# Optimization experiments

Hardware: AMD Instinct MI355X
Metric: run time of the kernel (lower is better)

Reference implementation:

```python
import jax, jax.numpy as jnp
from jax import lax
import numpy as np


def conv2d(x, w, b):
    # x: NCHW, w: OIHW, VALID padding, stride 1
    y = lax.conv_general_dilated(x, w, (1, 1), 'VALID',
                                 dimension_numbers=('NCHW', 'OIHW', 'NCHW'))
    return y + b[None, :, None, None]


def prelu(x, a):
    # per-channel PReLU, a: (C,)
    return jnp.where(x >= 0, x, a[None, :, None, None] * x)


def maxpool_ceil(x, k, s):
    # max pool with ceil_mode=True: pad right/bottom with -inf as needed
    H, W = x.shape[2], x.shape[3]
    def pad_amt(n):
        out = -(-(n - k) // s) + 1  # ceil
        return max(0, (out - 1) * s + k - n)
    ph, pw = pad_amt(H), pad_amt(W)
    return lax.reduce_window(x, -jnp.inf, lax.max,
                             (1, 1, k, k), (1, 1, s, s),
                             ((0, 0), (0, 0), (0, ph), (0, pw)))


def setup_inputs() -> dict:
    key = jax.random.key(0)
    ks = jax.random.split(key, 24)
    N = 2048
    x = jax.random.normal(ks[0], (N, 3, 48, 48), dtype=jnp.float32)

    def w_init(k, shape, fan_in):
        return jax.random.normal(k, shape, dtype=jnp.float32) * (1.0 / np.sqrt(fan_in))

    inp = {'x': x}
    inp['c1w'] = w_init(ks[1], (32, 3, 3, 3), 3 * 9)
    inp['c1b'] = jnp.zeros((32,), jnp.float32)
    inp['a1'] = jax.random.uniform(ks[2], (32,), jnp.float32, 0.1, 0.4)
    inp['c2w'] = w_init(ks[3], (64, 32, 3, 3), 32 * 9)
    inp['c2b'] = jnp.zeros((64,), jnp.float32)
    inp['a2'] = jax.random.uniform(ks[4], (64,), jnp.float32, 0.1, 0.4)
    inp['c3w'] = w_init(ks[5], (64, 64, 3, 3), 64 * 9)
    inp['c3b'] = jnp.zeros((64,), jnp.float32)
    inp['a3'] = jax.random.uniform(ks[6], (64,), jnp.float32, 0.1, 0.4)
    inp['c4w'] = w_init(ks[7], (128, 64, 2, 2), 64 * 4)
    inp['c4b'] = jnp.zeros((128,), jnp.float32)
    inp['a4'] = jax.random.uniform(ks[8], (128,), jnp.float32, 0.1, 0.4)
    inp['d5w'] = w_init(ks[9], (256, 1152), 1152)
    inp['d5b'] = jnp.zeros((256,), jnp.float32)
    inp['a5'] = jax.random.uniform(ks[10], (256,), jnp.float32, 0.1, 0.4)
    inp['d61w'] = w_init(ks[11], (2, 256), 256)
    inp['d61b'] = jnp.zeros((2,), jnp.float32)
    inp['d62w'] = w_init(ks[12], (4, 256), 256)
    inp['d62b'] = jnp.zeros((4,), jnp.float32)
    inp['d63w'] = w_init(ks[13], (10, 256), 256)
    inp['d63b'] = jnp.zeros((10,), jnp.float32)
    return inp


def reference(x, c1w, c1b, a1, c2w, c2b, a2, c3w, c3b, a3, c4w, c4b, a4,
              d5w, d5b, a5, d61w, d61b, d62w, d62b, d63w, d63b):
    h = prelu(conv2d(x, c1w, c1b), a1)          # [N,32,46,46]
    h = maxpool_ceil(h, 3, 2)                   # [N,32,23,23]
    h = prelu(conv2d(h, c2w, c2b), a2)          # [N,64,21,21]
    h = maxpool_ceil(h, 3, 2)                   # [N,64,10,10]
    h = prelu(conv2d(h, c3w, c3b), a3)          # [N,64,8,8]
    h = maxpool_ceil(h, 2, 2)                   # [N,64,4,4]
    h = prelu(conv2d(h, c4w, c4b), a4)          # [N,128,3,3]
    # torch: x.permute(0,3,2,1).contiguous().view(N,-1)
    h = jnp.transpose(h, (0, 3, 2, 1)).reshape(h.shape[0], -1)  # [N,1152]
    h = h @ d5w.T + d5b                         # [N,256]
    h = jnp.where(h >= 0, h, a5 * h)            # PReLU over features
    a = jax.nn.softmax(h @ d61w.T + d61b, axis=1)  # class probs [N,2]
    b = h @ d62w.T + d62b
    c = h @ d63w.T + d63b                       # landmarks [N,10]
    return (b, c, a)
```

## Files before the change

### kernel.cpp

```cpp
#include <hip/hip_runtime.h>
#include <hip/hip_bf16.h>
#include <hip/hip_fp16.h>
#include <stdint.h>

typedef short s16x8 __attribute__((ext_vector_type(8)));
typedef unsigned short u16x8 __attribute__((ext_vector_type(8)));
typedef _Float16 f16x8 __attribute__((ext_vector_type(8)));
typedef __fp16 h16x2 __attribute__((ext_vector_type(2)));
typedef float f32x4 __attribute__((ext_vector_type(4)));

__device__ __forceinline__ unsigned short f2h(float f) {
    __half h = __float2half(f);
    union { __half h; unsigned short u; } c; c.h = h; return c.u;
}
__device__ __forceinline__ float h2f(unsigned short u) {
    union { unsigned short u; __half h; } c; c.u = u; return __half2float(c.h);
}
__device__ __forceinline__ unsigned pkh(float a, float b) {
    union { h16x2 h; unsigned u; } c;
    c.h = __builtin_amdgcn_cvt_pkrtz(a, b);
    return c.u;
}

__global__ void k0_prep(const float* __restrict__ c2w, const float* __restrict__ c3w,
                        const float* __restrict__ c4w, const float* __restrict__ d5w,
                        unsigned short* __restrict__ w2, unsigned short* __restrict__ w3,
                        unsigned short* __restrict__ w4, unsigned short* __restrict__ w5) {
    int t = blockIdx.x * 256 + threadIdx.x;
    if (t < 18432) {
        int kpos = t / 2048, rem = t % 2048, oc = rem / 32, ic = rem % 32;
        w2[t] = f2h(c2w[(oc * 32 + ic) * 9 + kpos]);
        return;
    }
    t -= 18432;
    if (t < 36864) {
        int kpos = t / 4096, rem = t % 4096, oc = rem / 64, ic = rem % 64;
        w3[t] = f2h(c3w[(oc * 64 + ic) * 9 + kpos]);
        return;
    }
    t -= 36864;
    if (t < 32768) {
        int kpos = t / 8192, rem = t % 8192, oc = rem / 64, ic = rem % 64;
        w4[t] = f2h(c4w[(oc * 64 + ic) * 4 + kpos]);
        return;
    }
    t -= 32768;
    if (t < 294912) w5[t] = f2h(d5w[t]);
}

__global__ __launch_bounds__(256, 6)
void k1_conv1(const float* __restrict__ x, const float* __restrict__ c1w,
              const float* __restrict__ c1b, const float* __restrict__ a1,
              unsigned short* __restrict__ p1) {
    __shared__ unsigned short xstrip[1008];
    __shared__ unsigned short cbuf[230 * 40];
    __shared__ unsigned short wlds[1024];
    __shared__ float bls[32], als[32];

    const int n = blockIdx.x, tid = threadIdx.x;
    const int w = tid >> 6, lane = tid & 63, q = lane >> 4, l16 = lane & 15;

    for (int t = tid; t < 1024; t += 256) {
        int oc = t >> 5, k = t & 31;
        wlds[t] = (k < 27) ? f2h(c1w[oc * 27 + k]) : (unsigned short)0;
    }
    if (tid < 32) { bls[tid] = c1b[tid]; als[tid] = a1[tid]; }
    __syncthreads();

    f16x8 Wf[2];
    #pragma unroll
    for (int nt = 0; nt < 2; ++nt) {
        union { u16x8 u; f16x8 f; } cc;
        cc.u = *(const u16x8*)(wlds + (nt * 16 + l16) * 32 + q * 8);
        Wf[nt] = cc.f;
    }

    float bq[2][4], aq[2][4];
    #pragma unroll
    for (int nt = 0; nt < 2; ++nt)
    #pragma unroll
    for (int r = 0; r < 4; ++r) {
        bq[nt][r] = bls[nt * 16 + q * 4 + r];
        aq[nt][r] = als[nt * 16 + q * 4 + r];
    }

    int off[8];
    #pragma unroll
    for (int j = 0; j < 8; ++j) {
        int k = q * 8 + j;
        int kk = k < 27 ? k : 26;
        int ic = kk / 9, r9 = kk - ic * 9, ky = r9 / 3, kx = r9 - ky * 3;
        off[j] = ic * 336 + ky * 48 + kx;
    }

    auto do_pool = [&](int sp, int nprows, int kymax) {
        int ntask = nprows * 92;
        int t = tid;
        if (t < ntask) {
            int ocg = t & 3; unsigned r2 = (unsigned)t >> 2;
            int px = (int)(r2 % 23u), py_l = (int)(r2 / 23u);
            int kxmax = (px == 22) ? 2 : 3;
            int base = (2 * py_l * 46 + 2 * px) * 40 + ocg * 8;
            f16x8 mx;
            #pragma unroll
            for (int j = 0; j < 8; ++j) mx[j] = (_Float16)(-60000.f);
            #pragma unroll
            for (int ky = 0; ky < 3; ++ky) {
                if (ky < kymax) {
                    #pragma unroll
                    for (int kx = 0; kx < 3; ++kx) {
                        if (kx < kxmax) {
                            union { uint4 u; f16x8 f; } d;
                            d.u = *(const uint4*)&cbuf[base + (ky * 46 + kx) * 40];
                            mx = __builtin_elementwise_max(mx, d.f);
                        }
                    }
                }
            }
            union { f16x8 f; uint4 u; } o; o.f = mx;
            int py = 2 * sp + py_l;
            *(uint4*)&p1[n * 16928 + (py * 23 + px) * 32 + ocg * 8] = o.u;
        }
    };

    for (int s = 0; s < 12; ++s) {
        const int nrows = (s == 11) ? 2 : 5;
        const int P = 46 * nrows;
        const int ntiles = (P + 15) >> 4;
        const int xr0 = 4 * s;

        {
            int t4 = tid;
            if (t4 < 252) {
                int ic = t4 / 84;
                int rem4 = t4 * 4 - ic * 336;
                int rr = rem4 / 48, col = rem4 - rr * 48;
                int row = xr0 + rr; if (row > 47) row = 47;
                float4 f = *(const float4*)(x + n * 6912 + ic * 2304 + row * 48 + col);
                uint2 o; o.x = pkh(f.x, f.y); o.y = pkh(f.z, f.w);
                *(uint2*)&xstrip[t4 * 4] = o;
            }
        }
        if (s > 0) do_pool(s - 1, 2, 3);
        __syncthreads();

        for (int T = w; T < ntiles; T += 4) {
            int px = T * 16 + l16;
            int p = px < P ? px : P - 1;
            int ry = p / 46, cx = p - ry * 46;
            int basex = ry * 48 + cx;
            union { u16x8 u; f16x8 f; } xcc;
            #pragma unroll
            for (int j = 0; j < 8; ++j) xcc.u[j] = xstrip[basex + off[j]];
            f16x8 Xf = xcc.f;
            f32x4 acc[2] = {{0.f,0.f,0.f,0.f},{0.f,0.f,0.f,0.f}};
            #pragma unroll
            for (int nt = 0; nt < 2; ++nt)
                acc[nt] = __builtin_amdgcn_mfma_f32_16x16x32_f16(Wf[nt], Xf, acc[nt], 0, 0, 0);
            if (px < P) {
                #pragma unroll
                for (int nt = 0; nt < 2; ++nt) {
                    float v0 = acc[nt][0] + bq[nt][0];
                    float v1 = acc[nt][1] + bq[nt][1];
                    float v2 = acc[nt][2] + bq[nt][2];
                    float v3 = acc[nt][3] + bq[nt][3];
                    v0 = fmaxf(v0, 0.f) + aq[nt][0] * fminf(v0, 0.f);
                    v1 = fmaxf(v1, 0.f) + aq[nt][1] * fminf(v1, 0.f);
                    v2 = fmaxf(v2, 0.f) + aq[nt][2] * fminf(v2, 0.f);
                    v3 = fmaxf(v3, 0.f) + aq[nt][3] * fminf(v3, 0.f);
                    uint2 pk; pk.x = pkh(v0, v1); pk.y = pkh(v2, v3);
                    *(uint2*)&cbuf[px * 40 + nt * 16 + q * 4] = pk;
                }
            }
        }
        __syncthreads();
    }
    do_pool(11, 1, 2);
}

__global__ __launch_bounds__(256, 2)
void k23_fused(const unsigned short* __restrict__ p1, const unsigned short* __restrict__ w2,
               const float* __restrict__ c2b, const float* __restrict__ a2,
               const unsigned short* __restrict__ w3, const float* __restrict__ c3b,
               const float* __restrict__ a3, const unsigned short* __restrict__ w4,
               const float* __restrict__ c4b, const float* __restrict__ a4,
               unsigned short* __restrict__ flat) {
    __shared__ __align__(16) char smem[52128];
    unsigned short* xs    = (unsigned short*)(smem);
    unsigned short* c2s   = (unsigned short*)(smem + 16560);
    unsigned short* p2s   = (unsigned short*)(smem + 37728);
    unsigned short* c3buf = (unsigned short*)(smem);
    unsigned short* p3    = (unsigned short*)(smem + 8192);

    const int n = blockIdx.x, tid = threadIdx.x;
    const int w = tid >> 6, lane = tid & 63, q = lane >> 4, l16 = lane & 15;
    const unsigned short* p1n = p1 + n * 16928;

    const int npair = w & 1, tset = w >> 1;
    const int ocA = npair * 32 + l16, ocB = npair * 32 + 16 + l16;

    f16x8 B2[9][2];
    #pragma unroll
    for (int kp = 0; kp < 9; ++kp) {
        union { u16x8 u; f16x8 f; } c0, c1;
        c0.u = *(const u16x8*)(w2 + (kp * 64 + ocA) * 32 + q * 8);
        c1.u = *(const u16x8*)(w2 + (kp * 64 + ocB) * 32 + q * 8);
        B2[kp][0] = c0.f; B2[kp][1] = c1.f;
    }
    const float b2a = c2b[ocA], b2b = c2b[ocB];
    const float a2a = a2[ocA],  a2b = a2[ocB];

    auto stage = [&](int s) {
        int pr0 = 6 * s;
        for (int t = tid; t < 828; t += 256) {
            int pxl = t >> 2, c = t & 3;
            int rr = pxl / 23, colpx = pxl - rr * 23;
            int prow = pr0 + rr; if (prow > 22) prow = 22;
            uint4 d = ((const uint4*)p1n)[(prow * 23 + colpx) * 4 + c];
            ((uint4*)xs)[pxl * 5 + c] = d;
        }
    };

    auto conv2_strip = [&](int s) {
        const int nr = (s == 3) ? 3 : 7;
        const int P = 21 * nr;
        const int ntiles = (P + 15) >> 4;
        const int half = (ntiles + 1) >> 1;
        const int T0 = tset * half;
        const int T1 = (T0 + half) < ntiles ? (T0 + half) : ntiles;
        for (int T = T0; T < T1; ++T) {
            int m = T * 16 + l16;
            int p = m < P ? m : P - 1;
            int ry = p / 21, ox = p - ry * 21;
            const unsigned short* ab = xs + (ry * 23 + ox) * 40 + q * 8;
            f32x4 acc0 = {0.f, 0.f, 0.f, 0.f}, acc1 = {0.f, 0.f, 0.f, 0.f};
            #pragma unroll
            for (int kp = 0; kp < 9; ++kp) {
                int ky = kp / 3, kx = kp - ky * 3;
                union { u16x8 u; f16x8 f; } av;
                av.u = *(const u16x8*)(ab + (ky * 23 + kx) * 40);
                acc0 = __builtin_amdgcn_mfma_f32_16x16x32_f16(av.f, B2[kp][0], acc0, 0, 0, 0);
                acc1 = __builtin_amdgcn_mfma_f32_16x16x32_f16(av.f, B2[kp][1], acc1, 0, 0, 0);
            }
            int rowb = T * 16 + q * 4;
            #pragma unroll
            for (int r = 0; r < 4; ++r) {
                int row = rowb + r;
                if (row < P) {
                    float v0 = acc0[r] + b2a;
                    v0 = fmaxf(v0, 0.f) + a2a * fminf(v0, 0.f);
                    c2s[row * 72 + npair * 32 + l16] = f2h(v0);
                    float v1 = acc1[r] + b2b;
                    v1 = fmaxf(v1, 0.f) + a2b * fminf(v1, 0.f);
                    c2s[row * 72 + npair * 32 + 16 + l16] = f2h(v1);
                }
            }
        }
    };

    auto pool_strip = [&](int s) {
        int nprow = (s == 3) ? 1 : 3;
        int ntask = nprow * 80;
        if (tid < ntask) {
            int ocg = tid & 7; int r2 = tid >> 3;
            int px = r2 % 10, pyl = r2 / 10;
            int base = (2 * pyl * 21 + 2 * px) * 72 + ocg * 8;
            f16x8 mx;
            #pragma unroll
            for (int j = 0; j < 8; ++j) mx[j] = (_Float16)(-60000.f);
            #pragma unroll
            for (int ky = 0; ky < 3; ++ky)
            #pragma unroll
            for (int kx = 0; kx < 3; ++kx) {
                union { uint4 u; f16x8 f; } d;
                d.u = *(const uint4*)&c2s[base + (ky * 21 + kx) * 72];
                mx = __builtin_elementwise_max(mx, d.f);
            }
            union { f16x8 f; uint4 u; } o; o.f = mx;
            *(uint4*)&p2s[((3 * s + pyl) * 10 + px) * 72 + ocg * 8] = o.u;
        }
    };

    stage(0);
    __syncthreads();
    for (int s = 0; s < 4; ++s) {
        conv2_strip(s);
        __syncthreads();
        pool_strip(s);
        if (s < 3) stage(s + 1);
        __syncthreads();
    }

    {
        const int oc3 = w * 16 + l16;
        int mbase[4];
        #pragma unroll
        for (int j = 0; j < 4; ++j) {
            int px = j * 16 + l16;
            int oy = px >> 3, ox = px & 7;
            mbase[j] = (oy * 10 + ox) * 72 + q * 8;
        }
        f32x4 acc3[4];
        #pragma unroll
        for (int j = 0; j < 4; ++j) acc3[j] = f32x4{0.f, 0.f, 0.f, 0.f};
        union { u16x8 u; f16x8 f; } bc;
        bc.u = *(const u16x8*)(w3 + oc3 * 64 + q * 8);
        f16x8 B3c = bc.f;
        for (int c = 0; c < 18; ++c) {
            f16x8 B3n = B3c;
            if (c < 17) {
                int cn = c + 1;
                union { u16x8 u; f16x8 f; } bn;
                bn.u = *(const u16x8*)(w3 + ((cn >> 1) * 64 + oc3) * 64 + (cn & 1) * 32 + q * 8);
                B3n = bn.f;
            }
            int kp = c >> 1, ky = kp / 3, kx = kp - ky * 3;
            int aoff = (ky * 10 + kx) * 72 + (c & 1) * 32;
            #pragma unroll
            for (int j = 0; j < 4; ++j) {
                union { u16x8 u; f16x8 f; } av;
                av.u = *(const u16x8*)(p2s + mbase[j] + aoff);
                acc3[j] = __builtin_amdgcn_mfma_f32_16x16x32_f16(av.f, B3c, acc3[j], 0, 0, 0);
            }
            B3c = B3n;
        }
        float bias = c3b[oc3], al = a3[oc3];
        #pragma unroll
        for (int j = 0; j < 4; ++j)
        #pragma unroll
        for (int r = 0; r < 4; ++r) {
            int row = j * 16 + q * 4 + r;
            float val = acc3[j][r] + bias;
            val = fmaxf(val, 0.f) + al * fminf(val, 0.f);
            c3buf[row * 64 + oc3] = f2h(val);
        }
    }
    __syncthreads();

    if (tid < 128) {
        int ocg = tid & 7, r = tid >> 3;
        int py = r >> 2, pxo = r & 3;
        f16x8 mx;
        #pragma unroll
        for (int j = 0; j < 8; ++j) mx[j] = (_Float16)(-60000.f);
        #pragma unroll
        for (int ky = 0; ky < 2; ++ky)
        #pragma unroll
        for (int kx = 0; kx < 2; ++kx) {
            union { uint4 u; f16x8 f; } d;
            d.u = *(const uint4*)&c3buf[((py * 2 + ky) * 8 + pxo * 2 + kx) * 64 + ocg * 8];
            mx = __builtin_elementwise_max(mx, d.f);
        }
        union { f16x8 f; uint4 u; } o; o.f = mx;
        *(uint4*)&p3[r * 72 + ocg * 8] = o.u;
    }
    __syncthreads();

    {
        int px = l16 < 9 ? l16 : 8;
        int oy = px / 3, ox = px - oy * 3;
        const int mb4 = (oy * 4 + ox) * 72 + q * 8;
        const int oc4a = (w * 2) * 16 + l16, oc4b = (w * 2 + 1) * 16 + l16;
        f32x4 acc4[2] = {{0.f,0.f,0.f,0.f},{0.f,0.f,0.f,0.f}};
        f16x8 B4c[2];
        {
            union { u16x8 u; f16x8 f; } b0, b1;
            b0.u = *(const u16x8*)(w4 + oc4a * 64 + q * 8);
            b1.u = *(const u16x8*)(w4 + oc4b * 64 + q * 8);
            B4c[0] = b0.f; B4c[1] = b1.f;
        }
        for (int c = 0; c < 8; ++c) {
            f16x8 B4n[2] = {B4c[0], B4c[1]};
            if (c < 7) {
                int cn = c + 1;
                int boff = (cn >> 1) * 8192 + (cn & 1) * 32 + q * 8;
                union { u16x8 u; f16x8 f; } b0, b1;
                b0.u = *(const u16x8*)(w4 + boff + oc4a * 64);
                b1.u = *(const u16x8*)(w4 + boff + oc4b * 64);
                B4n[0] = b0.f; B4n[1] = b1.f;
            }
            int kp = c >> 1, ky = kp >> 1, kx = kp & 1;
            union { u16x8 u; f16x8 f; } av;
            av.u = *(const u16x8*)(p3 + mb4 + (ky * 4 + kx) * 72 + (c & 1) * 32);
            acc4[0] = __builtin_amdgcn_mfma_f32_16x16x32_f16(av.f, B4c[0], acc4[0], 0, 0, 0);
            acc4[1] = __builtin_amdgcn_mfma_f32_16x16x32_f16(av.f, B4c[1], acc4[1], 0, 0, 0);
            B4c[0] = B4n[0]; B4c[1] = B4n[1];
        }
        #pragma unroll
        for (int h = 0; h < 2; ++h) {
            int oc = h ? oc4b : oc4a;
            float bias = c4b[oc], al = a4[oc];
            #pragma unroll
            for (int r = 0; r < 4; ++r) {
                int row = q * 4 + r;
                if (row < 9) {
                    int hy = row / 3, wx = row - hy * 3;
                    float val = acc4[h][r] + bias;
                    val = fmaxf(val, 0.f) + al * fminf(val, 0.f);
                    flat[(unsigned)n * 1152u + (wx * 3 + hy) * 128 + oc] = f2h(val);
                }
            }
        }
    }
}

__global__ __launch_bounds__(256, 2)
void k5a_gemm(const unsigned short* __restrict__ flat, const unsigned short* __restrict__ w5,
              const float* __restrict__ d5b, const float* __restrict__ a5,
              unsigned short* __restrict__ h) {
    __shared__ float hbuf[4 * 16 * 128];
    const int blk = blockIdx.x, tid = threadIdx.x;
    const int w = tid >> 6, lane = tid & 63, q = lane >> 4, l16 = lane & 15;
    const int img0 = (blk >> 1) * 16, ocb = (blk & 1) * 128;
    const int img = img0 + l16;

    f32x4 acc[8];
    #pragma unroll
    for (int nt = 0; nt < 8; ++nt) acc[nt] = f32x4{0.f, 0.f, 0.f, 0.f};

    for (int cc = 0; cc < 9; ++cc) {
        int c = w * 9 + cc;
        int k0 = c * 32 + q * 8;
        union { u16x8 u; f16x8 f; } av;
        av.u = *(const u16x8*)(flat + (unsigned)img * 1152u + k0);
        #pragma unroll
        for (int nt = 0; nt < 8; ++nt) {
            int oc = ocb + nt * 16 + l16;
            union { u16x8 u; f16x8 f; } bv;
            bv.u = *(const u16x8*)(w5 + (unsigned)oc * 1152u + k0);
            acc[nt] = __builtin_amdgcn_mfma_f32_16x16x32_f16(av.f, bv.f, acc[nt], 0, 0, 0);
        }
    }
    #pragma unroll
    for (int nt = 0; nt < 8; ++nt)
    #pragma unroll
    for (int r = 0; r < 4; ++r) {
        int row = q * 4 + r;
        hbuf[(w * 16 + row) * 128 + nt * 16 + l16] = acc[nt][r];
    }
    __syncthreads();
    for (int t = tid; t < 1024; t += 256) {
        int im = t >> 6, oc2 = (t & 63) * 2;
        float s0 = hbuf[im * 128 + oc2]        + hbuf[(16 + im) * 128 + oc2]
                 + hbuf[(32 + im) * 128 + oc2] + hbuf[(48 + im) * 128 + oc2];
        float s1 = hbuf[im * 128 + oc2 + 1]        + hbuf[(16 + im) * 128 + oc2 + 1]
                 + hbuf[(32 + im) * 128 + oc2 + 1] + hbuf[(48 + im) * 128 + oc2 + 1];
        int oc = ocb + oc2;
        s0 += d5b[oc];     s0 = fmaxf(s0, 0.f) + a5[oc] * fminf(s0, 0.f);
        s1 += d5b[oc + 1]; s1 = fmaxf(s1, 0.f) + a5[oc + 1] * fminf(s1, 0.f);
        *(unsigned*)&h[(unsigned)(img0 + im) * 256u + oc] = pkh(s0, s1);
    }
}

__global__ __launch_bounds__(256, 2)
void k5b_head(const unsigned short* __restrict__ h,
              const float* __restrict__ d61w, const float* __restrict__ d61b,
              const float* __restrict__ d62w, const float* __restrict__ d62b,
              const float* __restrict__ d63w, const float* __restrict__ d63b,
              float* __restrict__ out) {
    __shared__ float hL[16 * 260];
    __shared__ float wl[16 * 260];
    __shared__ float lg[256];
    const int blk = blockIdx.x, tid = threadIdx.x;
    const int img0 = blk * 16;

    for (int t = tid; t < 512; t += 256) {
        int im = t >> 5, g = t & 31;
        union { uint4 u; f16x8 f; } d;
        d.u = *(const uint4*)&h[(unsigned)(img0 + im) * 256u + g * 8];
        float* dst = &hL[im * 260 + g * 8];
        #pragma unroll
        for (int j = 0; j < 8; ++j) dst[j] = (float)d.f[j];
    }
    {
        int o = tid >> 4, seg = tid & 15;
        const float* wrow = (o < 2) ? d61w + o * 256
                          : (o < 6) ? d62w + (o - 2) * 256
                          :           d63w + (o - 6) * 256;
        #pragma unroll
        for (int j = 0; j < 4; ++j)
            *(float4*)&wl[o * 260 + seg * 16 + j * 4] = ((const float4*)wrow)[seg * 4 + j];
    }
    __syncthreads();

    const int im = tid >> 4, o = tid & 15;
    {
        float bias = (o < 2) ? d61b[o] : (o < 6) ? d62b[o - 2] : d63b[o - 6];
        float s = bias;
        const float4* ha = (const float4*)&hL[im * 260];
        const float4* wa = (const float4*)&wl[o * 260];
        #pragma unroll 8
        for (int k = 0; k < 64; ++k) {
            float4 a = ha[k], b = wa[k];
            s += a.x * b.x + a.y * b.y + a.z * b.z + a.w * b.w;
        }
        lg[im * 16 + o] = s;
    }
    __syncthreads();
    {
        int gimg = img0 + im;
        float v = lg[im * 16 + o];
        if (o >= 2 && o < 6) {
            out[gimg * 4 + (o - 2)] = v;
        } else if (o >= 6) {
            out[8192 + gimg * 10 + (o - 6)] = v;
        } else {
            float l0 = lg[im * 16 + 0], l1 = lg[im * 16 + 1];
            float mx = fmaxf(l0, l1);
            float e0 = __expf(l0 - mx), e1 = __expf(l1 - mx);
            out[28672 + gimg * 2 + o] = (o == 0 ? e0 : e1) / (e0 + e1);
        }
    }
}

extern "C" void kernel_launch(void* const* d_in, const int* in_sizes, int n_in,
                              void* d_out, int out_size, void* d_ws, size_t ws_size,
                              hipStream_t stream) {
    (void)in_sizes; (void)n_in; (void)out_size; (void)ws_size;
    const float* x    = (const float*)d_in[0];
    const float* c1w  = (const float*)d_in[1];
    const float* c1b  = (const float*)d_in[2];
    const float* a1   = (const float*)d_in[3];
    const float* c2w  = (const float*)d_in[4];
    const float* c2b  = (const float*)d_in[5];
    const float* a2   = (const float*)d_in[6];
    const float* c3w  = (const float*)d_in[7];
    const float* c3b  = (const float*)d_in[8];
    const float* a3   = (const float*)d_in[9];
    const float* c4w  = (const float*)d_in[10];
    const float* c4b  = (const float*)d_in[11];
    const float* a4   = (const float*)d_in[12];
    const float* d5w  = (const float*)d_in[13];
    const float* d5b  = (const float*)d_in[14];
    const float* a5   = (const float*)d_in[15];
    const float* d61w = (const float*)d_in[16];
    const float* d61b = (const float*)d_in[17];
    const float* d62w = (const float*)d_in[18];
    const float* d62b = (const float*)d_in[19];
    const float* d63w = (const float*)d_in[20];
    const float* d63b = (const float*)d_in[21];

    char* ws = (char*)d_ws;
    unsigned short* p1    = (unsigned short*)(ws + 0);
    unsigned short* flat  = (unsigned short*)(ws + 69337088);
    unsigned short* h     = (unsigned short*)(ws + 74055680);
    unsigned short* w2    = (unsigned short*)(ws + 186777600);
    unsigned short* w3    = (unsigned short*)(ws + 186814464);
    unsigned short* w4    = (unsigned short*)(ws + 186888192);
    unsigned short* w5    = (unsigned short*)(ws + 186953728);

    k0_prep  <<<1496, 256, 0, stream>>>(c2w, c3w, c4w, d5w, w2, w3, w4, w5);
    k1_conv1 <<<2048, 256, 0, stream>>>(x, c1w, c1b, a1, p1);
    k23_fused<<<2048, 256, 0, stream>>>(p1, w2, c2b, a2, w3, c3b, a3, w4, c4b, a4, flat);
    k5a_gemm <<<256, 256, 0, stream>>>(flat, w5, d5b, a5, h);
    k5b_head <<<128, 256, 0, stream>>>(h, d61w, d61b, d62w, d62b, d63w, d63b,
                                       (float*)d_out);
}
```

Measured before the change: 296.9 us.

## Fuse dense GEMM into head kernel and shrink conv2 strip shared memory

The dense-5 GEMM and the head are merged into one kernel. Each block now computes all 256 outputs for 16 images with a full K loop, applies bias and PReLU, and writes to shared memory directly, which removes the global h buffer and one launch. In the conv2 stage, the padded strides (40, 72) become unpadded (32, 64), and the loop runs 5 strips of 5 rows instead of 4 strips of 7. This cuts shared memory so more blocks fit per CU and lets staging become a plain contiguous copy, at the risk of LDS bank conflicts. The fused kernel runs only 128 blocks with a long serial K loop, so it may underutilize the GPU.

```diff
diff --git a/kernel.cpp b/kernel.cpp
--- a/kernel.cpp
+++ b/kernel.cpp
@@ -12,9 +12,6 @@
 __device__ __forceinline__ unsigned short f2h(float f) {
     __half h = __float2half(f);
     union { __half h; unsigned short u; } c; c.h = h; return c.u;
-}
-__device__ __forceinline__ float h2f(unsigned short u) {
-    union { unsigned short u; __half h; } c; c.u = u; return __half2float(c.h);
 }
 __device__ __forceinline__ unsigned pkh(float a, float b) {
     union { h16x2 h; unsigned u; } c;
@@ -185,10 +182,10 @@
                const float* __restrict__ a3, const unsigned short* __restrict__ w4,
                const float* __restrict__ c4b, const float* __restrict__ a4,
                unsigned short* __restrict__ flat) {
-    __shared__ __align__(16) char smem[52128];
+    __shared__ __align__(16) char smem[36544];
     unsigned short* xs    = (unsigned short*)(smem);
-    unsigned short* c2s   = (unsigned short*)(smem + 16560);
-    unsigned short* p2s   = (unsigned short*)(smem + 37728);
+    unsigned short* c2s   = (unsigned short*)(smem + 10304);
+    unsigned short* p2s   = (unsigned short*)(smem + 23744);
     unsigned short* c3buf = (unsigned short*)(smem);
     unsigned short* p3    = (unsigned short*)(smem + 8192);
 
@@ -211,34 +208,25 @@
     const float a2a = a2[ocA],  a2b = a2[ocB];
 
     auto stage = [&](int s) {
-        int pr0 = 6 * s;
-        for (int t = tid; t < 828; t += 256) {
-            int pxl = t >> 2, c = t & 3;
-            int rr = pxl / 23, colpx = pxl - rr * 23;
-            int prow = pr0 + rr; if (prow > 22) prow = 22;
-            uint4 d = ((const uint4*)p1n)[(prow * 23 + colpx) * 4 + c];
-            ((uint4*)xs)[pxl * 5 + c] = d;
-        }
+        const uint4* src = ((const uint4*)p1n) + 368 * s;
+        for (int t = tid; t < 644; t += 256) ((uint4*)xs)[t] = src[t];
     };
 
-    auto conv2_strip = [&](int s) {
-        const int nr = (s == 3) ? 3 : 7;
-        const int P = 21 * nr;
-        const int ntiles = (P + 15) >> 4;
-        const int half = (ntiles + 1) >> 1;
+    auto conv2_strip = [&]() {
+        const int P = 105, ntiles = 7, half = 4;
         const int T0 = tset * half;
         const int T1 = (T0 + half) < ntiles ? (T0 + half) : ntiles;
         for (int T = T0; T < T1; ++T) {
             int m = T * 16 + l16;
             int p = m < P ? m : P - 1;
             int ry = p / 21, ox = p - ry * 21;
-            const unsigned short* ab = xs + (ry * 23 + ox) * 40 + q * 8;
+            const unsigned short* ab = xs + (ry * 23 + ox) * 32 + q * 8;
             f32x4 acc0 = {0.f, 0.f, 0.f, 0.f}, acc1 = {0.f, 0.f, 0.f, 0.f};
             #pragma unroll
             for (int kp = 0; kp < 9; ++kp) {
                 int ky = kp / 3, kx = kp - ky * 3;
                 union { u16x8 u; f16x8 f; } av;
-                av.u = *(const u16x8*)(ab + (ky * 23 + kx) * 40);
+                av.u = *(const u16x8*)(ab + (ky * 23 + kx) * 32);
                 acc0 = __builtin_amdgcn_mfma_f32_16x16x32_f16(av.f, B2[kp][0], acc0, 0, 0, 0);
                 acc1 = __builtin_amdgcn_mfma_f32_16x16x32_f16(av.f, B2[kp][1], acc1, 0, 0, 0);
             }
@@ -249,22 +237,20 @@
                 if (row < P) {
                     float v0 = acc0[r] + b2a;
                     v0 = fmaxf(v0, 0.f) + a2a * fminf(v0, 0.f);
-                    c2s[row * 72 + npair * 32 + l16] = f2h(v0);
+                    c2s[row * 64 + npair * 32 + l16] = f2h(v0);
                     float v1 = acc1[r] + b2b;
                     v1 = fmaxf(v1, 0.f) + a2b * fminf(v1, 0.f);
-                    c2s[row * 72 + npair * 32 + 16 + l16] = f2h(v1);
+                    c2s[row * 64 + npair * 32 + 16 + l16] = f2h(v1);
                 }
             }
         }
     };
 
     auto pool_strip = [&](int s) {
-        int nprow = (s == 3) ? 1 : 3;
-        int ntask = nprow * 80;
-        if (tid < ntask) {
+        if (tid < 160) {
             int ocg = tid & 7; int r2 = tid >> 3;
             int px = r2 % 10, pyl = r2 / 10;
-            int base = (2 * pyl * 21 + 2 * px) * 72 + ocg * 8;
+            int base = (2 * pyl * 21 + 2 * px) * 64 + ocg * 8;
             f16x8 mx;
             #pragma unroll
             for (int j = 0; j < 8; ++j) mx[j] = (_Float16)(-60000.f);
@@ -273,21 +259,21 @@
             #pragma unroll
             for (int kx = 0; kx < 3; ++kx) {
                 union { uint4 u; f16x8 f; } d;
-                d.u = *(const uint4*)&c2s[base + (ky * 21 + kx) * 72];
+                d.u = *(const uint4*)&c2s[base + (ky * 21 + kx) * 64];
                 mx = __builtin_elementwise_max(mx, d.f);
             }
             union { f16x8 f; uint4 u; } o; o.f = mx;
-            *(uint4*)&p2s[((3 * s + pyl) * 10 + px) * 72 + ocg * 8] = o.u;
+            *(uint4*)&p2s[((2 * s + pyl) * 10 + px) * 64 + ocg * 8] = o.u;
         }
     };
 
     stage(0);
     __syncthreads();
-    for (int s = 0; s < 4; ++s) {
-        conv2_strip(s);
+    for (int s = 0; s < 5; ++s) {
+        conv2_strip();
         __syncthreads();
         pool_strip(s);
-        if (s < 3) stage(s + 1);
+        if (s < 4) stage(s + 1);
         __syncthreads();
     }
 
@@ -298,7 +284,7 @@
         for (int j = 0; j < 4; ++j) {
             int px = j * 16 + l16;
             int oy = px >> 3, ox = px & 7;
-            mbase[j] = (oy * 10 + ox) * 72 + q * 8;
+            mbase[j] = (oy * 10 + ox) * 64 + q * 8;
         }
         f32x4 acc3[4];
         #pragma unroll
@@ -315,7 +301,7 @@
                 B3n = bn.f;
             }
             int kp = c >> 1, ky = kp / 3, kx = kp - ky * 3;
-            int aoff = (ky * 10 + kx) * 72 + (c & 1) * 32;
+            int aoff = (ky * 10 + kx) * 64 + (c & 1) * 32;
             #pragma unroll
             for (int j = 0; j < 4; ++j) {
                 union { u16x8 u; f16x8 f; } av;
@@ -352,14 +338,14 @@
             mx = __builtin_elementwise_max(mx, d.f);
         }
         union { f16x8 f; uint4 u; } o; o.f = mx;
-        *(uint4*)&p3[r * 72 + ocg * 8] = o.u;
+        *(uint4*)&p3[r * 64 + ocg * 8] = o.u;
     }
     __syncthreads();
 
     {
         int px = l16 < 9 ? l16 : 8;
         int oy = px / 3, ox = px - oy * 3;
-        const int mb4 = (oy * 4 + ox) * 72 + q * 8;
+        const int mb4 = (oy * 4 + ox) * 64 + q * 8;
         const int oc4a = (w * 2) * 16 + l16, oc4b = (w * 2 + 1) * 16 + l16;
         f32x4 acc4[2] = {{0.f,0.f,0.f,0.f},{0.f,0.f,0.f,0.f}};
         f16x8 B4c[2];
@@ -381,7 +367,7 @@
             }
             int kp = c >> 1, ky = kp >> 1, kx = kp & 1;
             union { u16x8 u; f16x8 f; } av;
-            av.u = *(const u16x8*)(p3 + mb4 + (ky * 4 + kx) * 72 + (c & 1) * 32);
+            av.u = *(const u16x8*)(p3 + mb4 + (ky * 4 + kx) * 64 + (c & 1) * 32);
             acc4[0] = __builtin_amdgcn_mfma_f32_16x16x32_f16(av.f, B4c[0], acc4[0], 0, 0, 0);
             acc4[1] = __builtin_amdgcn_mfma_f32_16x16x32_f16(av.f, B4c[1], acc4[1], 0, 0, 0);
             B4c[0] = B4n[0]; B4c[1] = B4n[1];
@@ -405,55 +391,8 @@
 }
 
 __global__ __launch_bounds__(256, 2)
-void k5a_gemm(const unsigned short* __restrict__ flat, const unsigned short* __restrict__ w5,
+void k5_fused(const unsigned short* __restrict__ flat, const unsigned short* __restrict__ w5,
               const float* __restrict__ d5b, const float* __restrict__ a5,
-              unsigned short* __restrict__ h) {
-    __shared__ float hbuf[4 * 16 * 128];
-    const int blk = blockIdx.x, tid = threadIdx.x;
-    const int w = tid >> 6, lane = tid & 63, q = lane >> 4, l16 = lane & 15;
-    const int img0 = (blk >> 1) * 16, ocb = (blk & 1) * 128;
-    const int img = img0 + l16;
-
-    f32x4 acc[8];
-    #pragma unroll
-    for (int nt = 0; nt < 8; ++nt) acc[nt] = f32x4{0.f, 0.f, 0.f, 0.f};
-
-    for (int cc = 0; cc < 9; ++cc) {
-        int c = w * 9 + cc;
-        int k0 = c * 32 + q * 8;
-        union { u16x8 u; f16x8 f; } av;
-        av.u = *(const u16x8*)(flat + (unsigned)img * 1152u + k0);
-        #pragma unroll
-        for (int nt = 0; nt < 8; ++nt) {
-            int oc = ocb + nt * 16 + l16;
-            union { u16x8 u; f16x8 f; } bv;
-            bv.u = *(const u16x8*)(w5 + (unsigned)oc * 1152u + k0);
-            acc[nt] = __builtin_amdgcn_mfma_f32_16x16x32_f16(av.f, bv.f, acc[nt], 0, 0, 0);
-        }
-    }
-    #pragma unroll
-    for (int nt = 0; nt < 8; ++nt)
-    #pragma unroll
-    for (int r = 0; r < 4; ++r) {
-        int row = q * 4 + r;
-        hbuf[(w * 16 + row) * 128 + nt * 16 + l16] = acc[nt][r];
-    }
-    __syncthreads();
-    for (int t = tid; t < 1024; t += 256) {
-        int im = t >> 6, oc2 = (t & 63) * 2;
-        float s0 = hbuf[im * 128 + oc2]        + hbuf[(16 + im) * 128 + oc2]
-                 + hbuf[(32 + im) * 128 + oc2] + hbuf[(48 + im) * 128 + oc2];
-        float s1 = hbuf[im * 128 + oc2 + 1]        + hbuf[(16 + im) * 128 + oc2 + 1]
-                 + hbuf[(32 + im) * 128 + oc2 + 1] + hbuf[(48 + im) * 128 + oc2 + 1];
-        int oc = ocb + oc2;
-        s0 += d5b[oc];     s0 = fmaxf(s0, 0.f) + a5[oc] * fminf(s0, 0.f);
-        s1 += d5b[oc + 1]; s1 = fmaxf(s1, 0.f) + a5[oc + 1] * fminf(s1, 0.f);
-        *(unsigned*)&h[(unsigned)(img0 + im) * 256u + oc] = pkh(s0, s1);
-    }
-}
-
-__global__ __launch_bounds__(256, 2)
-void k5b_head(const unsigned short* __restrict__ h,
               const float* __restrict__ d61w, const float* __restrict__ d61b,
               const float* __restrict__ d62w, const float* __restrict__ d62b,
               const float* __restrict__ d63w, const float* __restrict__ d63b,
@@ -462,15 +401,37 @@
     __shared__ float wl[16 * 260];
     __shared__ float lg[256];
     const int blk = blockIdx.x, tid = threadIdx.x;
+    const int w = tid >> 6, lane = tid & 63, q = lane >> 4, l16 = lane & 15;
     const int img0 = blk * 16;
-
-    for (int t = tid; t < 512; t += 256) {
-        int im = t >> 5, g = t & 31;
-        union { uint4 u; f16x8 f; } d;
-        d.u = *(const uint4*)&h[(unsigned)(img0 + im) * 256u + g * 8];
-        float* dst = &hL[im * 260 + g * 8];
-        #pragma unroll
-        for (int j = 0; j < 8; ++j) dst[j] = (float)d.f[j];
+    const int img = img0 + l16;
+
+    f32x4 acc[4];
+    #pragma unroll
+    for (int nt = 0; nt < 4; ++nt) acc[nt] = f32x4{0.f, 0.f, 0.f, 0.f};
+
+    for (int c = 0; c < 36; ++c) {
+        int k0 = c * 32 + q * 8;
+        union { u16x8 u; f16x8 f; } av;
+        av.u = *(const u16x8*)(flat + (unsigned)img * 1152u + k0);
+        #pragma unroll
+        for (int nt = 0; nt < 4; ++nt) {
+            int oc = w * 64 + nt * 16 + l16;
+            union { u16x8 u; f16x8 f; } bv;
+            bv.u = *(const u16x8*)(w5 + (unsigned)oc * 1152u + k0);
+            acc[nt] = __builtin_amdgcn_mfma_f32_16x16x32_f16(av.f, bv.f, acc[nt], 0, 0, 0);
+        }
+    }
+    #pragma unroll
+    for (int nt = 0; nt < 4; ++nt) {
+        int oc = w * 64 + nt * 16 + l16;
+        float bias = d5b[oc], al = a5[oc];
+        #pragma unroll
+        for (int r = 0; r < 4; ++r) {
+            int im = q * 4 + r;
+            float v = acc[nt][r] + bias;
+            v = fmaxf(v, 0.f) + al * fminf(v, 0.f);
+            hL[im * 260 + oc] = v;
+        }
     }
     {
         int o = tid >> 4, seg = tid & 15;
@@ -543,7 +504,6 @@
     char* ws = (char*)d_ws;
     unsigned short* p1    = (unsigned short*)(ws + 0);
     unsigned short* flat  = (unsigned short*)(ws + 69337088);
-    unsigned short* h     = (unsigned short*)(ws + 74055680);
     unsigned short* w2    = (unsigned short*)(ws + 186777600);
     unsigned short* w3    = (unsigned short*)(ws + 186814464);
     unsigned short* w4    = (unsigned short*)(ws + 186888192);
@@ -552,7 +512,6 @@
     k0_prep  <<<1496, 256, 0, stream>>>(c2w, c3w, c4w, d5w, w2, w3, w4, w5);
     k1_conv1 <<<2048, 256, 0, stream>>>(x, c1w, c1b, a1, p1);
     k23_fused<<<2048, 256, 0, stream>>>(p1, w2, c2b, a2, w3, c3b, a3, w4, c4b, a4, flat);
-    k5a_gemm <<<256, 256, 0, stream>>>(flat, w5, d5b, a5, h);
-    k5b_head <<<128, 256, 0, stream>>>(h, d61w, d61b, d62w, d62b, d63w, d63b,
-                                       (float*)d_out);
-}
+    k5_fused <<<128, 256, 0, stream>>>(flat, w5, d5b, a5, d61w, d61b, d62w, d62b,
+                                       d63w, d63b, (float*)d_out);
+}
```

Result: no change. 294.5 us (-0.8%).
